# Performance work log

Hardware: AMD Instinct MI355X
Metric: run time of the kernel (lower is better)

Reference implementation:

```python
import jax, jax.numpy as jnp
import numpy as np

N_POINTS = 100000
N_EVENTS = 1000000
N_PAIRS = 100000      # node_pair_samples
N_RIEMANN = 128       # riemann_samples
INIT_BETA = 0.025
NON_EVENT_W = 1.0
EPS = 1e-6            # torch PairwiseDistance default eps (added to the difference)


def setup_inputs() -> dict:
    key = jax.random.key(0)
    ks = jax.random.split(key, 8)
    # learned parameters
    beta = jnp.full((1, 1), INIT_BETA, jnp.float32)
    z0 = jax.random.uniform(ks[0], (N_POINTS, 2), jnp.float32, -0.025, 0.025)
    v0 = jax.random.uniform(ks[1], (N_POINTS, 2), jnp.float32, -0.025, 0.025)
    a0 = jnp.zeros((N_POINTS, 2), jnp.float32)  # a0 is referenced by step(); zero -> constant-velocity
    # event data: (u, v, event_time)
    u = jax.random.randint(ks[2], (N_EVENTS,), 0, N_POINTS)
    v = jax.random.randint(ks[3], (N_EVENTS,), 0, N_POINTS)
    event_times = jax.random.uniform(ks[4], (N_EVENTS,), jnp.float32, 0.0, 1.0)
    # sampled non-event node pairs (stand-in for randperm over triu indices)
    pair_u = jax.random.randint(ks[5], (N_PAIRS,), 0, N_POINTS)
    pair_v = jax.random.randint(ks[6], (N_PAIRS,), 0, N_POINTS)
    pair_v = jnp.where(pair_v == pair_u, (pair_v + 1) % N_POINTS, pair_v)
    t0 = jnp.float32(0.0)
    tn = jnp.float32(1.0)
    return {"beta": beta, "z0": z0, "v0": v0, "a0": a0,
            "u": u, "v": v, "event_times": event_times,
            "pair_u": pair_u, "pair_v": pair_v, "t0": t0, "tn": tn}


def reference(beta, z0, v0, a0, u, v, event_times, pair_u, pair_v, t0, tn):
    b = beta[0, 0]
    # ---- event intensity: sum_e (beta - ||z_u(t_e) - z_v(t_e)||) ----
    te = event_times[:, None]                                  # [E,1]
    zu = z0[u] + v0[u] * te + 0.5 * a0[u] * te ** 2            # [E,2]
    zv = z0[v] + v0[v] * te + 0.5 * a0[v] * te ** 2            # [E,2]
    d_ev = jnp.sqrt(jnp.sum((zu - zv + EPS) ** 2, axis=-1))    # [E]
    event_intensity = b * event_times.shape[0] - jnp.sum(d_ev)
    # ---- non-event intensity: Riemann sum of exp(beta - d(t)) over sampled pairs ----
    ts = t0 + (jnp.arange(N_RIEMANN, dtype=jnp.float32) / N_RIEMANN) * (tn - t0)  # [T] left Riemann
    dt = (tn - t0) / N_RIEMANN
    dz = z0[pair_u] - z0[pair_v]                               # [P,2]
    dv = v0[pair_u] - v0[pair_v]
    da = a0[pair_u] - a0[pair_v]
    tt = ts[None, :, None]                                     # [1,T,1]
    diff = dz[:, None, :] + dv[:, None, :] * tt + 0.5 * da[:, None, :] * tt ** 2 + EPS  # [P,T,2]
    d_ne = jnp.sqrt(jnp.sum(diff ** 2, axis=-1))               # [P,T]
    non_event_intensity = jnp.sum(jnp.exp(b - d_ne)) * dt
    return event_intensity - NON_EVENT_W * non_event_intensity
```

## Files before the change

kernel.cpp:

```cpp
#include <hip/hip_runtime.h>

#define N_POINTS   100000
#define N_EVENTS   1000000
#define N_PAIRS    100000
#define N_RIEMANN  128
#define EPS_F      1e-6f
#define NON_EVENT_W 1.0f

constexpr int BLOCK = 256;
constexpr int EV_BLOCKS = 1024;
constexpr int PAIR_BLOCKS = (N_PAIRS + BLOCK - 1) / BLOCK;
constexpr int TOTAL_BLOCKS = EV_BLOCKS + PAIR_BLOCKS;

__device__ __forceinline__ float block_reduce_sum(float v) {
    #pragma unroll
    for (int off = 32; off > 0; off >>= 1)
        v += __shfl_down(v, off, 64);
    __shared__ float smem[BLOCK / 64];
    const int lane = threadIdx.x & 63;
    const int wid  = threadIdx.x >> 6;
    if (lane == 0) smem[wid] = v;
    __syncthreads();
    float r = 0.f;
    if (threadIdx.x == 0) {
        #pragma unroll
        for (int i = 0; i < BLOCK / 64; ++i) r += smem[i];
    }
    return r;
}

__global__ __launch_bounds__(BLOCK) void partials_kernel(
    const float*  __restrict__ beta,
    const float2* __restrict__ z0,
    const float2* __restrict__ v0,
    const float2* __restrict__ a0,
    const int*    __restrict__ eu,
    const int*    __restrict__ ev,
    const float*  __restrict__ et,
    const int*    __restrict__ pu,
    const int*    __restrict__ pv,
    const float*  __restrict__ t0p,
    const float*  __restrict__ tnp,
    float*        __restrict__ partials)
{
    float acc = 0.f;
    const int b = blockIdx.x;

    if (b < EV_BLOCKS) {
        for (int i = b * BLOCK + threadIdx.x; i < N_EVENTS; i += EV_BLOCKS * BLOCK) {
            const float te = et[i];
            const int iu = eu[i];
            const int iv = ev[i];
            const float2 zu = z0[iu], zvv = z0[iv];
            const float2 vu = v0[iu], vvv = v0[iv];
            const float2 au = a0[iu], avv = a0[iv];
            const float h = 0.5f * te * te;
            const float dx = (zu.x - zvv.x) + (vu.x - vvv.x) * te + (au.x - avv.x) * h + EPS_F;
            const float dy = (zu.y - zvv.y) + (vu.y - vvv.y) * te + (au.y - avv.y) * h + EPS_F;
            acc -= sqrtf(dx * dx + dy * dy);
        }
    } else {
        const int p = (b - EV_BLOCKS) * BLOCK + threadIdx.x;
        if (p < N_PAIRS) {
            const float t0v = t0p[0];
            const float tnv = tnp[0];
            const float dt  = (tnv - t0v) * (1.0f / N_RIEMANN);
            const float bb  = beta[0];
            const int iu = pu[p];
            const int iv = pv[p];
            const float2 zuu = z0[iu], zvv = z0[iv];
            const float2 vuu = v0[iu], vvv = v0[iv];
            const float2 auu = a0[iu], avv = a0[iv];
            const float dzx = zuu.x - zvv.x, dzy = zuu.y - zvv.y;
            const float dvx = vuu.x - vvv.x, dvy = vuu.y - vvv.y;
            const float dax = auu.x - avv.x, day = auu.y - avv.y;
            float s = 0.f;
            #pragma unroll 4
            for (int k = 0; k < N_RIEMANN; ++k) {
                const float t = t0v + (float)k * (1.0f / N_RIEMANN) * (tnv - t0v);
                const float h = 0.5f * t * t;
                const float dx = dzx + dvx * t + dax * h + EPS_F;
                const float dy = dzy + dvy * t + day * h + EPS_F;
                s += __expf(bb - sqrtf(dx * dx + dy * dy));
            }
            acc = -NON_EVENT_W * dt * s;
        }
    }

    const float r = block_reduce_sum(acc);
    if (threadIdx.x == 0) partials[blockIdx.x] = r;
}

__global__ __launch_bounds__(BLOCK) void reduce_kernel(
    const float* __restrict__ partials,
    const float* __restrict__ beta,
    float*       __restrict__ out)
{
    float acc = 0.f;
    for (int i = threadIdx.x; i < TOTAL_BLOCKS; i += BLOCK) acc += partials[i];
    const float r = block_reduce_sum(acc);
    if (threadIdx.x == 0) out[0] = beta[0] * (float)N_EVENTS + r;
}

extern "C" void kernel_launch(void* const* d_in, const int* in_sizes, int n_in,
                              void* d_out, int out_size, void* d_ws, size_t ws_size,
                              hipStream_t stream) {
    const float*  beta = (const float*)d_in[0];
    const float2* z0   = (const float2*)d_in[1];
    const float2* v0   = (const float2*)d_in[2];
    const float2* a0   = (const float2*)d_in[3];
    const int*    eu   = (const int*)d_in[4];
    const int*    ev   = (const int*)d_in[5];
    const float*  et   = (const float*)d_in[6];
    const int*    pu   = (const int*)d_in[7];
    const int*    pv   = (const int*)d_in[8];
    const float*  t0p  = (const float*)d_in[9];
    const float*  tnp  = (const float*)d_in[10];

    float* partials = (float*)d_ws;
    float* out      = (float*)d_out;

    partials_kernel<<<TOTAL_BLOCKS, BLOCK, 0, stream>>>(
        beta, z0, v0, a0, eu, ev, et, pu, pv, t0p, tnp, partials);
    reduce_kernel<<<1, BLOCK, 0, stream>>>(partials, beta, out);
}
```

Measured before the change: 125.9 us.

## Interleave point state into AoS buffer, one event per thread, atomic final reduce

A prep kernel packs z0, v0 and a0 into one interleaved float4 buffer, so each endpoint gather reads 32 contiguous bytes instead of touching three separate arrays. The prep kernel also initialises the output with the beta term. The event phase now maps one event per thread over a full grid. The separate reduce kernel is replaced by per-block atomicAdd into the output, and exp(beta) is factored out of the Riemann loop. This adds an extra launch and a pass over the points, and float atomics make the summation order nondeterministic.

```diff
diff --git a/kernel.cpp b/kernel.cpp
--- a/kernel.cpp
+++ b/kernel.cpp
@@ -8,9 +8,11 @@
 #define NON_EVENT_W 1.0f
 
 constexpr int BLOCK = 256;
-constexpr int EV_BLOCKS = 1024;
+constexpr int PREP_BLOCKS = (N_POINTS + BLOCK - 1) / BLOCK;
+constexpr int EV_BLOCKS   = (N_EVENTS + BLOCK - 1) / BLOCK;
 constexpr int PAIR_BLOCKS = (N_PAIRS + BLOCK - 1) / BLOCK;
-constexpr int TOTAL_BLOCKS = EV_BLOCKS + PAIR_BLOCKS;
+constexpr int MAIN_BLOCKS = EV_BLOCKS + PAIR_BLOCKS;
+
 
 __device__ __forceinline__ float block_reduce_sum(float v) {
     #pragma unroll
@@ -29,11 +31,31 @@
     return r;
 }
 
-__global__ __launch_bounds__(BLOCK) void partials_kernel(
-    const float*  __restrict__ beta,
+__global__ __launch_bounds__(BLOCK) void prep_kernel(
     const float2* __restrict__ z0,
     const float2* __restrict__ v0,
     const float2* __restrict__ a0,
+    const float*  __restrict__ beta,
+    float4*       __restrict__ pts,
+    float*        __restrict__ out)
+{
+    const int i = blockIdx.x * BLOCK + threadIdx.x;
+    if (i < N_POINTS) {
+        const float2 z = z0[i], v = v0[i], a = a0[i];
+        pts[2 * i]     = make_float4(z.x, z.y, v.x, v.y);
+        pts[2 * i + 1] = make_float4(a.x, a.y, 0.f, 0.f);
+    }
+    if (blockIdx.x == 0 && threadIdx.x == 0)
+        out[0] = beta[0] * (float)N_EVENTS;
+}
+
+template <bool INTERLEAVED>
+__global__ __launch_bounds__(BLOCK) void main_kernel(
+    const float4* __restrict__ pts,
+    const float2* __restrict__ z0,
+    const float2* __restrict__ v0,
+    const float2* __restrict__ a0,
+    const float*  __restrict__ beta,
     const int*    __restrict__ eu,
     const int*    __restrict__ ev,
     const float*  __restrict__ et,
@@ -41,23 +63,38 @@
     const int*    __restrict__ pv,
     const float*  __restrict__ t0p,
     const float*  __restrict__ tnp,
-    float*        __restrict__ partials)
+    float*        __restrict__ out)
 {
     float acc = 0.f;
     const int b = blockIdx.x;
 
     if (b < EV_BLOCKS) {
-        for (int i = b * BLOCK + threadIdx.x; i < N_EVENTS; i += EV_BLOCKS * BLOCK) {
-            const float te = et[i];
+        const int i = b * BLOCK + threadIdx.x;
+        if (i < N_EVENTS) {
             const int iu = eu[i];
             const int iv = ev[i];
-            const float2 zu = z0[iu], zvv = z0[iv];
-            const float2 vu = v0[iu], vvv = v0[iv];
-            const float2 au = a0[iu], avv = a0[iv];
+            const float te = et[i];
+            float dzx, dzy, dvx, dvy, dax, day;
+            if (INTERLEAVED) {
+                const float4 u0 = pts[2 * iu];
+                const float4 u1 = pts[2 * iu + 1];
+                const float4 w0 = pts[2 * iv];
+                const float4 w1 = pts[2 * iv + 1];
+                dzx = u0.x - w0.x; dzy = u0.y - w0.y;
+                dvx = u0.z - w0.z; dvy = u0.w - w0.w;
+                dax = u1.x - w1.x; day = u1.y - w1.y;
+            } else {
+                const float2 zu = z0[iu], zv = z0[iv];
+                const float2 vu = v0[iu], vv = v0[iv];
+                const float2 au = a0[iu], av = a0[iv];
+                dzx = zu.x - zv.x; dzy = zu.y - zv.y;
+                dvx = vu.x - vv.x; dvy = vu.y - vv.y;
+                dax = au.x - av.x; day = au.y - av.y;
+            }
             const float h = 0.5f * te * te;
-            const float dx = (zu.x - zvv.x) + (vu.x - vvv.x) * te + (au.x - avv.x) * h + EPS_F;
-            const float dy = (zu.y - zvv.y) + (vu.y - vvv.y) * te + (au.y - avv.y) * h + EPS_F;
-            acc -= sqrtf(dx * dx + dy * dy);
+            const float dx = dzx + dvx * te + dax * h + EPS_F;
+            const float dy = dzy + dvy * te + day * h + EPS_F;
+            acc = -sqrtf(dx * dx + dy * dy);
         }
     } else {
         const int p = (b - EV_BLOCKS) * BLOCK + threadIdx.x;
@@ -68,12 +105,24 @@
             const float bb  = beta[0];
             const int iu = pu[p];
             const int iv = pv[p];
-            const float2 zuu = z0[iu], zvv = z0[iv];
-            const float2 vuu = v0[iu], vvv = v0[iv];
-            const float2 auu = a0[iu], avv = a0[iv];
-            const float dzx = zuu.x - zvv.x, dzy = zuu.y - zvv.y;
-            const float dvx = vuu.x - vvv.x, dvy = vuu.y - vvv.y;
-            const float dax = auu.x - avv.x, day = auu.y - avv.y;
+            float dzx, dzy, dvx, dvy, dax, day;
+            if (INTERLEAVED) {
+                const float4 u0 = pts[2 * iu];
+                const float4 u1 = pts[2 * iu + 1];
+                const float4 w0 = pts[2 * iv];
+                const float4 w1 = pts[2 * iv + 1];
+                dzx = u0.x - w0.x; dzy = u0.y - w0.y;
+                dvx = u0.z - w0.z; dvy = u0.w - w0.w;
+                dax = u1.x - w1.x; day = u1.y - w1.y;
+            } else {
+                const float2 zu = z0[iu], zv = z0[iv];
+                const float2 vu = v0[iu], vv = v0[iv];
+                const float2 au = a0[iu], av = a0[iv];
+                dzx = zu.x - zv.x; dzy = zu.y - zv.y;
+                dvx = vu.x - vv.x; dvy = vu.y - vv.y;
+                dax = au.x - av.x; day = au.y - av.y;
+            }
+            const float eb = __expf(bb);
             float s = 0.f;
             #pragma unroll 4
             for (int k = 0; k < N_RIEMANN; ++k) {
@@ -81,25 +130,14 @@
                 const float h = 0.5f * t * t;
                 const float dx = dzx + dvx * t + dax * h + EPS_F;
                 const float dy = dzy + dvy * t + day * h + EPS_F;
-                s += __expf(bb - sqrtf(dx * dx + dy * dy));
+                s += __expf(-sqrtf(dx * dx + dy * dy));
             }
-            acc = -NON_EVENT_W * dt * s;
+            acc = -NON_EVENT_W * dt * eb * s;
         }
     }
 
     const float r = block_reduce_sum(acc);
-    if (threadIdx.x == 0) partials[blockIdx.x] = r;
-}
-
-__global__ __launch_bounds__(BLOCK) void reduce_kernel(
-    const float* __restrict__ partials,
-    const float* __restrict__ beta,
-    float*       __restrict__ out)
-{
-    float acc = 0.f;
-    for (int i = threadIdx.x; i < TOTAL_BLOCKS; i += BLOCK) acc += partials[i];
-    const float r = block_reduce_sum(acc);
-    if (threadIdx.x == 0) out[0] = beta[0] * (float)N_EVENTS + r;
+    if (threadIdx.x == 0) atomicAdd(out, r);
 }
 
 extern "C" void kernel_launch(void* const* d_in, const int* in_sizes, int n_in,
@@ -117,10 +155,17 @@
     const float*  t0p  = (const float*)d_in[9];
     const float*  tnp  = (const float*)d_in[10];
 
-    float* partials = (float*)d_ws;
-    float* out      = (float*)d_out;
+    float*  out = (float*)d_out;
+    float4* pts = (float4*)d_ws;
+    const bool interleave = (ws_size >= (size_t)(2 * N_POINTS) * sizeof(float4));
 
-    partials_kernel<<<TOTAL_BLOCKS, BLOCK, 0, stream>>>(
-        beta, z0, v0, a0, eu, ev, et, pu, pv, t0p, tnp, partials);
-    reduce_kernel<<<1, BLOCK, 0, stream>>>(partials, beta, out);
+    if (interleave) {
+        prep_kernel<<<PREP_BLOCKS, BLOCK, 0, stream>>>(z0, v0, a0, beta, pts, out);
+        main_kernel<true><<<MAIN_BLOCKS, BLOCK, 0, stream>>>(
+            pts, z0, v0, a0, beta, eu, ev, et, pu, pv, t0p, tnp, out);
+    } else {
+        prep_kernel<<<1, BLOCK, 0, stream>>>(z0, v0, a0, beta, pts, out);
+        main_kernel<false><<<MAIN_BLOCKS, BLOCK, 0, stream>>>(
+            pts, z0, v0, a0, beta, eu, ev, et, pu, pv, t0p, tnp, out);
+    }
 }
```

After: 156.5 us. +24.2%, slower.
